# Kernel tuning notes

Measured on AMD Instinct MI355X. Metric: run time of the kernel, lower is better.

## Reference

```python
import jax, jax.numpy as jnp
import numpy as np

NUM_ENTITY = 500000
NUM_RELATION = 6000
NUM_WORD = 200000
D = 100          # entity_dim == word_dim
L = 3            # num_layer
B, E, F, Q = 16, 2000, 8000, 20
PAGERANK_LAMBDA = 0.8
FACT_SCALE = 3.0
VERY_NEG = -1e11
VERY_SMALL = 1e-10


def setup_inputs() -> dict:
    key = jax.random.key(0)
    ks = jax.random.split(key, 24)
    s = 0.05
    return {
        'local_entity': jax.random.randint(ks[0], (B, E), 0, NUM_ENTITY),
        'kb_fact_rel': jax.random.randint(ks[1], (B, F), 0, NUM_RELATION),
        'kb_head': jax.random.randint(ks[2], (B, F), 0, E),
        'kb_tail': jax.random.randint(ks[3], (B, F), 0, E),
        'query_text': jax.random.randint(ks[4], (B, Q), 0, NUM_WORD),
        'q2e_adj_mat': jax.random.uniform(ks[5], (B, E, 1)),
        'entity_table': jax.random.normal(ks[6], (NUM_ENTITY + 1, D)) * s,
        'rel_table': jax.random.normal(ks[7], (NUM_RELATION + 1, D)) * s,
        'word_table': jax.random.normal(ks[8], (NUM_WORD + 1, D)) * s,
        'rel_lin_w': jax.random.normal(ks[9], (D, D)) * s,
        'rel_lin_b': jnp.zeros((D,)),
        'lstm_wih': jax.random.normal(ks[10], (4 * D, D)) * s,
        'lstm_whh': jax.random.normal(ks[11], (4 * D, D)) * s,
        'lstm_bih': jnp.zeros((4 * D,)),
        'lstm_bhh': jnp.zeros((4 * D,)),
        'q2e_w': jax.random.normal(ks[12], (L, D, D)) * s,
        'q2e_b': jnp.zeros((L, D)),
        'e2q_w': jax.random.normal(ks[13], (L, D, 3 * D)) * s,
        'e2q_b': jnp.zeros((L, D)),
        'e2e_w': jax.random.normal(ks[14], (L, D, 3 * D)) * s,
        'e2e_b': jnp.zeros((L, D)),
        'head_w': jax.random.normal(ks[15], (L, D, D)) * s,
        'head_b': jnp.zeros((L, D)),
        'tail_w': jax.random.normal(ks[16], (L, D, D)) * s,
        'tail_b': jnp.zeros((L, D)),
        'self_w': jax.random.normal(ks[17], (L, D, D)) * s,
        'self_b': jnp.zeros((L, D)),
        'score_w': jax.random.normal(ks[18], (1, D)) * s,
        'score_b': jnp.zeros((1,)),
    }


def _lstm(x, wih, whh, bih, bhh):
    # x: (B, Q, D); torch LSTM gate order i,f,g,o
    b = x.shape[0]
    h0 = jnp.zeros((b, D), x.dtype)

    def step(carry, xt):
        h, c = carry
        g = xt @ wih.T + h @ whh.T + bih + bhh
        i, f, gg, o = jnp.split(g, 4, axis=-1)
        c = jax.nn.sigmoid(f) * c + jax.nn.sigmoid(i) * jnp.tanh(gg)
        h = jax.nn.sigmoid(o) * jnp.tanh(c)
        return (h, c), h

    (h, _), hs = jax.lax.scan(step, (h0, h0), x.transpose(1, 0, 2))
    return hs.transpose(1, 0, 2), h


def _gather(x, idx):
    # sparse_bmm(entity2fact, x): out[b,f] = x[b, head[b,f]]
    return jnp.take_along_axis(x, idx[:, :, None], axis=1)


def _scatter(x, idx, num):
    # sparse_bmm(fact2entity, x): segment-sum facts onto tail entities
    b, f, d = x.shape
    flat = (idx + jnp.arange(b)[:, None] * num).reshape(-1)
    return jax.ops.segment_sum(x.reshape(b * f, d), flat, num_segments=b * num).reshape(b, num, d)


def reference(local_entity, kb_fact_rel, kb_head, kb_tail, query_text, q2e_adj_mat,
              entity_table, rel_table, word_table, rel_lin_w, rel_lin_b,
              lstm_wih, lstm_whh, lstm_bih, lstm_bhh,
              q2e_w, q2e_b, e2q_w, e2q_b, e2e_w, e2e_b,
              head_w, head_b, tail_w, tail_b, self_w, self_b, score_w, score_b):
    div = float(np.sqrt(D))
    q_mask = (query_text != NUM_WORD).astype(jnp.float32)
    e_mask = (local_entity != NUM_ENTITY).astype(jnp.float32)

    # query LSTM encoding
    q_emb = word_table[query_text]                                   # (B,Q,D)
    q_hidden, q_last = _lstm(q_emb, lstm_wih, lstm_whh, lstm_bih, lstm_bhh)
    query_node_emb = q_last[:, None, :]                              # (B,1,D)

    # fact embeddings from relations
    fact_emb = rel_table[kb_fact_rel] @ rel_lin_w.T + rel_lin_b      # (B,F,D)

    # fact-to-query attention weights (softmax over query words)
    sim = jnp.einsum('bqd,bfd->bqf', q_hidden, fact_emb) / div
    sim = jax.nn.softmax(sim + (1.0 - q_mask)[:, :, None] * VERY_NEG, axis=1)
    att = jnp.einsum('bqf,bqd->bfd', sim, q_hidden)                  # (B,F,D)
    Wf = jnp.sum(att * fact_emb, axis=2) / div                       # (B,F)
    W_tilde = jnp.exp(Wf - Wf.max(axis=1, keepdims=True))
    e2f_softmax = jnp.clip(_scatter(W_tilde[:, :, None], kb_head, E)[:, :, 0], VERY_SMALL, None)

    local_entity_emb = entity_table[local_entity]                    # (B,E,D)
    pagerank_f = q2e_adj_mat[:, :, 0]                                # (B,E)

    for i in range(L):
        q2e_emb = jnp.broadcast_to(query_node_emb @ q2e_w[i].T + q2e_b[i], (B, E, D))
        # entity -> fact (gather heads)
        e2f = jax.nn.relu(fact_emb @ self_w[i].T + self_b[i] +
                          _gather(local_entity_emb @ head_w[i].T + head_b[i], kb_head))
        e2f = e2f * (W_tilde[:, :, None] * _gather((pagerank_f / e2f_softmax)[:, :, None], kb_head))
        # fact -> entity (scatter to tails)
        f2e = jax.nn.relu(local_entity_emb @ self_w[i].T + self_b[i] +
                          FACT_SCALE * _scatter(e2f @ tail_w[i].T + tail_b[i], kb_tail, E))
        # pagerank propagation
        pr = _scatter(_gather(pagerank_f[:, :, None], kb_head), kb_tail, E)[:, :, 0]
        pagerank_f = PAGERANK_LAMBDA * pr + (1.0 - PAGERANK_LAMBDA) * pagerank_f
        # k=3 concat -> e2q / e2e updates
        nxt = jnp.concatenate([local_entity_emb, q2e_emb, f2e], axis=2)   # (B,E,3D)
        query_node_emb = jnp.einsum('be,bed->bd', pagerank_f, nxt @ e2q_w[i].T + e2q_b[i])[:, None, :]
        local_entity_emb = jax.nn.relu(nxt @ e2e_w[i].T + e2e_b[i])

    score = (local_entity_emb @ score_w.T + score_b)[:, :, 0]
    return score + (1.0 - e_mask) * VERY_NEG
```

## Files before the change

kernel.cpp:

```cpp
#include <hip/hip_runtime.h>
#include <math.h>

namespace {

typedef unsigned short u16;
typedef short bf16x8 __attribute__((ext_vector_type(8)));
typedef float f32x4 __attribute__((ext_vector_type(4)));

constexpr int B = 16, E = 2000, F = 8000, Q = 20, D = 100, NLAYER = 3;
constexpr int NUM_ENTITY_C = 500000;
constexpr int NREL1 = 6001;
constexpr int SK = 128;
constexpr int WFSZ = 28 * 64 * 8;
constexpr int SST = 120;
constexpr float PAGERANK_LAMBDA = 0.8f;
constexpr float FACT_SCALE = 3.0f;
constexpr float VERY_NEG = -100000000000.0f;
constexpr float VERY_SMALL = 1e-10f;

__device__ __forceinline__ float sigf(float x) { return 1.0f / (1.0f + __expf(-x)); }

__device__ __forceinline__ short f2bf(float f) {
    union { float f; unsigned int u; } c; c.f = f;
    unsigned int u = c.u + 0x7FFF + ((c.u >> 16) & 1);
    return (short)(u >> 16);
}
__device__ __forceinline__ float bf2f(u16 s) {
    union { unsigned int u; float f; } c; c.u = ((unsigned int)s) << 16;
    return c.f;
}

__global__ void wprep_kernel(const float* __restrict__ rel_lin_w,
                             const float* __restrict__ self_w, const float* __restrict__ head_w,
                             const float* __restrict__ tail_w, const float* __restrict__ e2e_w,
                             u16* __restrict__ WF)
{
    int m = blockIdx.y;
    int ns = blockIdx.x;
    int n = ns >> 2, s = ns & 3;
    int lane = threadIdx.x;
    const float* W; int ldW = D, kofs = 0; float scale = 1.f;
    if (m == 0) { W = rel_lin_w; }
    else {
        int L = (m - 1) / 5, t = (m - 1) % 5;
        if (t == 0)      { W = self_w + (size_t)L * D * D; }
        else if (t == 1) { W = head_w + (size_t)L * D * D; }
        else if (t == 2) { W = tail_w + (size_t)L * D * D; scale = FACT_SCALE; }
// ... 63 lines not shown
            for (int n = 0; n < 2; ++n) {
                bf16x8 qb = *reinterpret_cast<const bf16x8*>(
                    qhB + ((size_t)(b * 8 + n * 4 + s) * 64 + lane) * 8);
                acc[n] = __builtin_amdgcn_mfma_f32_16x16x32_bf16(af[s], qb, acc[n], 0, 0, 0);
            }
        }
        const bool v1 = lrow < (Q - 16);
#pragma unroll
        for (int r = 0; r < 4; ++r) {
            float s0 = acc[0][r] * 0.1f;
            float s1 = acc[1][r] * 0.1f;
            float m = v1 ? fmaxf(s0, s1) : s0;
#pragma unroll
            for (int d = 1; d < 16; d <<= 1) m = fmaxf(m, __shfl_xor(m, d));
            float e0 = __expf(s0 - m);
            float e1 = v1 ? __expf(s1 - m) : 0.f;
            float sum = e0 + e1;
            float wsum = fmaf(e0, s0, e1 * s1);
#pragma unroll
            for (int d = 1; d < 16; d <<= 1) {
                sum += __shfl_xor(sum, d);
                wsum += __shfl_xor(wsum, d);
            }
            if (lrow == 0) {
                int orow = chunk * 16 + lkg * 4 + r;
                float wtl = __expf(wsum / sum);
                wt[orow] = wtl;
                atomicAdd(&e2fsm[headAbs[orow]], wtl);
            }
        }
    }
}

__global__ __launch_bounds__(256, 2) void mm2pipe(
    const u16* __restrict__ RELp, const int* __restrict__ srel,
    const u16* __restrict__ embp, const int* __restrict__ shead,
    const u16* __restrict__ WF1, const u16* __restrict__ WF2,
    const float* __restrict__ b1, const float* __restrict__ b2,
    const float* __restrict__ wtv, const float* __restrict__ prv,
    u16* __restrict__ outp, int nrows)
{
    __shared__ __align__(16) u16 stage[4][16][SST];
    const int lane = threadIdx.x & 63;
    const int lrow = lane & 15, lkg = lane >> 4;
    const int wslot = threadIdx.x >> 6;
    const int nch = (nrows + 15) >> 4;

    const int g = blockIdx.x & 7;
    const int lb = blockIdx.x >> 3;
    const int nchg = nch >> 3;
    const int cbase = g * nchg;
    const int wvg = lb * 4 + wslot;
    const int nwvg = 64 * 4;

    bf16x8 w1[7][4];
#pragma unroll
    for (int n = 0; n < 7; ++n)
#pragma unroll
        for (int s = 0; s < 4; ++s)
            w1[n][s] = *reinterpret_cast<const bf16x8*>(WF1 + ((size_t)(n * 4 + s) * 64 + lane) * 8);

    auto loadA = [&](int ch, bf16x8* f1, bf16x8* f2) {
        int row = ch * 16 + lrow;
        int ar = row < nrows ? row : nrows - 1;
        const u16* s1p = RELp + (size_t)srel[ar] * SK;
        const u16* s2p = embp + (size_t)shead[ar] * SK;
#pragma unroll
        for (int s = 0; s < 4; ++s) {
            f1[s] = *reinterpret_cast<const bf16x8*>(s1p + s * 32 + lkg * 8);
            f2[s] = *reinterpret_cast<const bf16x8*>(s2p + s * 32 + lkg * 8);
        }
    };

    int chunk = cbase + wvg;
    const int cend = cbase + nchg;
    if (chunk >= cend) return;
    bf16x8 cf1[4], cf2[4];
    loadA(chunk, cf1, cf2);
    while (true) {
        const int nxt = chunk + nwvg;
        const bool more = nxt < cend;
        bf16x8 nf1[4], nf2[4];
        if (more) loadA(nxt, nf1, nf2);

        f32x4 acc[7];
#pragma unroll
        for (int n = 0; n < 7; ++n) acc[n] = (f32x4){0.f, 0.f, 0.f, 0.f};
#pragma unroll
        for (int s = 0; s < 4; ++s) {
#pragma unroll
            for (int n = 0; n < 7; ++n)
                acc[n] = __builtin_amdgcn_mfma_f32_16x16x32_bf16(cf1[s], w1[n][s], acc[n], 0, 0, 0);
#pragma unroll
            for (int n = 0; n < 7; ++n) {
                bf16x8 w2 = *reinterpret_cast<const bf16x8*>(
                    WF2 + ((size_t)(n * 4 + s) * 64 + lane) * 8);
                acc[n] = __builtin_amdgcn_mfma_f32_16x16x32_bf16(cf2[s], w2, acc[n], 0, 0, 0);
            }
        }

        const int rb = chunk * 16 + lkg * 4;
#pragma unroll
        for (int r = 0; r < 4; ++r) {
            const int orow = rb + r;
            const int grow = orow < nrows ? orow : nrows - 1;
            const float rsv = wtv[grow] * prv[shead[grow]];
#pragma unroll
            for (int n = 0; n < 7; ++n) {
                const int col = n * 16 + lrow;
                float v = 0.f;
                if (col < D) {
                    v = acc[n][r] + b1[col] + b2[col];
                    v = fmaxf(v, 0.f) * rsv;
                }
                stage[wslot][lkg * 4 + r][col] = (u16)f2bf(v);
            }
        }
#pragma unroll
        for (int idx = lane; idx < 16 * 13; idx += 64) {
            int rr = idx / 13, cc = idx - rr * 13;
            int orow = chunk * 16 + rr;
            bf16x8 v = *reinterpret_cast<const bf16x8*>(&stage[wslot][rr][cc * 8]);
            if (orow < nrows)
                *reinterpret_cast<bf16x8*>(outp + (size_t)orow * SK + cc * 8) = v;
        }

        if (!more) break;
#pragma unroll
        for (int s = 0; s < 4; ++s) { cf1[s] = nf1[s]; cf2[s] = nf2[s]; }
        chunk = nxt;
    }
}

template<int A1S, int A2S, int EPI, bool OUTBF, bool PR>
__global__ __launch_bounds__(256, 2) void mm2(
    const void* __restrict__ A1p, const int* __restrict__ idx1, int lda1,
    const void* __restrict__ A2p, const int* __restrict__ idx2,
    const u16* __restrict__ WF1, const u16* __restrict__ WF2,
    const float* __restrict__ b1, const float* __restrict__ b2,
    const float* __restrict__ vq,
    const float* __restrict__ wtv, const float* __restrict__ prv,
    const int* __restrict__ row_start,
    const float* __restrict__ prOld, const int* __restrict__ sheadv,
    float* __restrict__ prNew,
    void* __restrict__ outp, int nrows)
{
    __shared__ __align__(16) u16 stage[4][16][SST];
    const int lane = threadIdx.x & 63;
    const int lrow = lane & 15, lkg = lane >> 4;
    const int wslot = threadIdx.x >> 6;
    const int wv = blockIdx.x * (blockDim.x >> 6) + wslot;
    const int nwv = gridDim.x * (blockDim.x >> 6);
    const int nch = (nrows + 15) >> 4;

    bf16x8 w1[7][4];
#pragma unroll
    for (int n = 0; n < 7; ++n)
#pragma unroll
        for (int s = 0; s < 4; ++s)
            w1[n][s] = *reinterpret_cast<const bf16x8*>(WF1 + ((size_t)(n * 4 + s) * 64 + lane) * 8);

    for (int chunk = wv; chunk < nch; chunk += nwv) {
        const int row = chunk * 16 + lrow;
        const int ar = row < nrows ? row : nrows - 1;

        bf16x8 af1[4];
        if (A1S == 0) {
            const u16* src = (const u16*)A1p + (size_t)ar * SK;
#pragma unroll
            for (int s = 0; s < 4; ++s)
                af1[s] = *reinterpret_cast<const bf16x8*>(src + s * 32 + lkg * 8);
        } else if (A1S == 1) {
            const u16* src = (const u16*)A1p + (size_t)idx1[ar] * SK;
#pragma unroll
            for (int s = 0; s < 4; ++s)
                af1[s] = *reinterpret_cast<const bf16x8*>(src + s * 32 + lkg * 8);
        } else {
            const float* arow = (const float*)A1p + (size_t)ar * lda1;
#pragma unroll
            for (int s = 0; s < 4; ++s) {
                const int k0 = s * 32 + lkg * 8;
                float tv[8];
                if (k0 + 8 <= D) {
                    float4 v0 = *reinterpret_cast<const float4*>(arow + k0);
                    float4 v1 = *reinterpret_cast<const float4*>(arow + k0 + 4);
                    tv[0]=v0.x; tv[1]=v0.y; tv[2]=v0.z; tv[3]=v0.w;
                    tv[4]=v1.x; tv[5]=v1.y; tv[6]=v1.z; tv[7]=v1.w;
                } else {
#pragma unroll
                    for (int j = 0; j < 8; ++j) tv[j] = (k0 + j < D) ? arow[k0 + j] : 0.f;
                }
                bf16x8 f;
#pragma unroll
                for (int j = 0; j < 8; ++j) f[j] = f2bf(tv[j]);
                af1[s] = f;
            }
        }

        int s0 = 0, s1 = 0;
        if (A2S == 2) { s0 = row_start[ar]; s1 = row_start[ar + 1]; }

        bf16x8 af2[4];
        if (A2S == 1) {
            const u16* src = (const u16*)A2p + (size_t)idx2[ar] * SK;
#pragma unroll
            for (int s = 0; s < 4; ++s)
                af2[s] = *reinterpret_cast<const bf16x8*>(src + s * 32 + lkg * 8);
        } else if (A2S == 3) {
            const u16* src = (const u16*)A2p + (size_t)ar * SK;
#pragma unroll
            for (int s = 0; s < 4; ++s)
                af2[s] = *reinterpret_cast<const bf16x8*>(src + s * 32 + lkg * 8);
        }

        f32x4 acc[7];
#pragma unroll
        for (int n = 0; n < 7; ++n) acc[n] = (f32x4){0.f, 0.f, 0.f, 0.f};
#pragma unroll
        for (int s = 0; s < 4; ++s) {
#pragma unroll
            for (int n = 0; n < 7; ++n)
                acc[n] = __builtin_amdgcn_mfma_f32_16x16x32_bf16(af1[s], w1[n][s], acc[n], 0, 0, 0);
            if (A2S == 1 || A2S == 3) {
#pragma unroll
                for (int n = 0; n < 7; ++n) {
                    bf16x8 w2 = *reinterpret_cast<const bf16x8*>(
                        WF2 + ((size_t)(n * 4 + s) * 64 + lane) * 8);
                    acc[n] = __builtin_amdgcn_mfma_f32_16x16x32_bf16(af2[s], w2, acc[n], 0, 0, 0);
                }
            } else if (A2S == 2) {
                float a2f[8];
#pragma unroll
                for (int j = 0; j < 8; ++j) a2f[j] = 0.f;
                for (int i = s0; i < s1; ++i) {
                    bf16x8 v = *reinterpret_cast<const bf16x8*>(
                        (const u16*)A2p + (size_t)i * SK + s * 32 + lkg * 8);
#pragma unroll
                    for (int j = 0; j < 8; ++j) a2f[j] += bf2f((u16)v[j]);
                }
                bf16x8 fsum;
#pragma unroll
                for (int j = 0; j < 8; ++j) fsum[j] = f2bf(a2f[j]);
#pragma unroll
                for (int n = 0; n < 7; ++n) {
                    bf16x8 w2 = *reinterpret_cast<const bf16x8*>(
                        WF2 + ((size_t)(n * 4 + s) * 64 + lane) * 8);
                    acc[n] = __builtin_amdgcn_mfma_f32_16x16x32_bf16(fsum, w2, acc[n], 0, 0, 0);
                }
            }
        }
        if (PR && A2S == 2) {
            if (lkg == 0 && row < nrows) {
                float a = 0.f;
                for (int i = s0; i < s1; ++i) a += prOld[sheadv[i]];
                prNew[row] = PAGERANK_LAMBDA * a + (1.0f - PAGERANK_LAMBDA) * prOld[row];
            }
        }

        const int rb = chunk * 16 + lkg * 4;
        const int bb = (chunk * 16) / E;
#pragma unroll
        for (int r = 0; r < 4; ++r) {
            const int orow = rb + r;
            const int grow = orow < nrows ? orow : nrows - 1;
            float rsv = 1.f, cntf = 0.f;
            if (EPI == 1) rsv = wtv[grow] * prv[idx2[grow]];
            if (EPI == 2) cntf = (float)(row_start[grow + 1] - row_start[grow]);
            float scr = 0.f;
#pragma unroll
            for (int n = 0; n < 7; ++n) {
                const int col = n * 16 + lrow;
                float v = 0.f;
                if (col < D) {
                    v = acc[n][r];
                    if (b1) v += b1[col];
                    if (EPI == 1) v += b2[col];
                    if (EPI == 2) v += FACT_SCALE * cntf * b2[col];
                    if (EPI == 3 || EPI == 4) v += vq[bb * D + col];
                    if (EPI != 0) v = fmaxf(v, 0.f);
                    if (EPI == 1) v *= rsv;
                }
                if (EPI == 4) {
                    if (col < D) scr = fmaf(v, b2[col], scr);
                } else if (OUTBF) {
                    stage[wslot][lkg * 4 + r][col] = (u16)f2bf(v);
                } else if (col < D && orow < nrows) {
                    ((float*)outp)[(size_t)orow * D + col] = v;
                }
            }
            if (EPI == 4) {
                scr += __shfl_xor(scr, 1);
                scr += __shfl_xor(scr, 2);
                scr += __shfl_xor(scr, 4);
                scr += __shfl_xor(scr, 8);
                if (lrow == 0 && orow < nrows) {
                    float s = scr + prOld[0] +
                              ((sheadv[orow] != NUM_ENTITY_C) ? 0.f : VERY_NEG);
                    ((float*)outp)[orow] = s;
                }
            }
        }
        if (OUTBF && EPI != 4) {
#pragma unroll
            for (int idx = lane; idx < 16 * 13; idx += 64) {
                int rr = idx / 13, cc = idx - rr * 13;
                int orow = chunk * 16 + rr;
                bf16x8 v = *reinterpret_cast<const bf16x8*>(&stage[wslot][rr][cc * 8]);
                if (orow < nrows)
                    *reinterpret_cast<bf16x8*>((u16*)outp + (size_t)orow * SK + cc * 8) = v;
            }
        }
    }
}

__global__ __launch_bounds__(512) void gatesx_kernel(
    const int* __restrict__ qtext, const float* __restrict__ wtab,
    const float* __restrict__ wih, const float* __restrict__ bih,
    const float* __restrict__ bhh, float* __restrict__ gx)
{
    int row = blockIdx.x;
    int t = threadIdx.x;
    __shared__ __align__(16) float xs[D];
    if (t < D) xs[t] = wtab[(size_t)qtext[row] * D + t];
    __syncthreads();
    if (t < 4 * D) {
        const float4* w4 = reinterpret_cast<const float4*>(wih + (size_t)t * D);
        const float4* x4 = reinterpret_cast<const float4*>(xs);
        float a0 = 0.f, a1 = 0.f, a2 = 0.f, a3 = 0.f;
#pragma unroll
        for (int k = 0; k < 25; ++k) {
            float4 wv = w4[k]; float4 xv = x4[k];
            a0 = fmaf(wv.x, xv.x, a0); a1 = fmaf(wv.y, xv.y, a1);
            a2 = fmaf(wv.z, xv.z, a2); a3 = fmaf(wv.w, xv.w, a3);
        }
        gx[(size_t)row * (4 * D) + t] = a0 + a1 + a2 + a3 + bih[t] + bhh[t];
    }
}

__global__ __launch_bounds__(512) void lstmrec_kernel(
    const float* __restrict__ gx, const float* __restrict__ whh,
    float* __restrict__ q_hidden, float* __restrict__ qne)
{
    int b = blockIdx.x, t = threadIdx.x;
// ... 5 lines not shown
        const float4* wr = reinterpret_cast<const float4*>(whh + (size_t)t * D);
#pragma unroll
        for (int k = 0; k < 25; ++k) w[k] = wr[k];
    }
    if (t < D) { h[t] = 0.f; cst[t] = 0.f; }
    __syncthreads();
    for (int step = 0; step < Q; ++step) {
        if (t < 4 * D) {
            const float4* h4 = reinterpret_cast<const float4*>(h);
            float a0 = 0.f, a1 = 0.f, a2 = 0.f, a3 = 0.f;
#pragma unroll
            for (int k = 0; k < 25; ++k) {
                float4 hv = h4[k];
                a0 = fmaf(w[k].x, hv.x, a0); a1 = fmaf(w[k].y, hv.y, a1);
                a2 = fmaf(w[k].z, hv.z, a2); a3 = fmaf(w[k].w, hv.w, a3);
            }
            g[t] = a0 + a1 + a2 + a3 + gx[((size_t)b * Q + step) * (4 * D) + t];
        }
        __syncthreads();
        if (t < D) {
            float gi = g[t], gf = g[t + D], gg = g[t + 2 * D], go = g[t + 3 * D];
            float cn = sigf(gf) * cst[t] + sigf(gi) * tanhf(gg);
            float hn = sigf(go) * tanhf(cn);
            cst[t] = cn; h[t] = hn;
            q_hidden[((size_t)b * Q + step) * D + t] = hn;
            if (step == Q - 1) qne[b * D + t] = hn;
        }
        __syncthreads();
    }
}

__global__ void idxabs_kernel(const int* __restrict__ kb_head, const int* __restrict__ kb_tail,
                              int* __restrict__ headAbs, int* __restrict__ tailAbs,
                              int* __restrict__ counts)
{
    int r = blockIdx.x * 256 + threadIdx.x;
    if (r < B * F) {
        int b = r / F;
        headAbs[r] = b * E + kb_head[r];
        int t = b * E + kb_tail[r];
        tailAbs[r] = t;
        atomicAdd(&counts[t], 1);
    }
}

__global__ __launch_bounds__(1024) void scan_kernel(const int* __restrict__ counts,
                                                    int* __restrict__ row_start,
                                                    int* __restrict__ cursor)
{
    __shared__ int part[1024];
    int t = threadIdx.x;
    int base = t * 32;
    int local[32];
    int s = 0;
#pragma unroll
    for (int i = 0; i < 32; ++i) {
        int idx = base + i;
        int v = (idx < B * E) ? counts[idx] : 0;
        local[i] = s; s += v;
    }
    part[t] = s;
    __syncthreads();
    for (int off = 1; off < 1024; off <<= 1) {
        int v = (t >= off) ? part[t - off] : 0;
        __syncthreads();
        if (t >= off) part[t] += v;
        __syncthreads();
    }
    int prev = (t > 0) ? part[t - 1] : 0;
#pragma unroll
    for (int i = 0; i < 32; ++i) {
        int idx = base + i;
        if (idx < B * E) { int rs = prev + local[i]; row_start[idx] = rs; cursor[idx] = rs; }
    }
    if (t == 1023) row_start[B * E] = part[1023];
}

__global__ void fillsprep_kernel(const int* __restrict__ tailAbs, int* __restrict__ cursor,
                                 const int* __restrict__ headAbs, const int* __restrict__ frel,
                                 const float* __restrict__ wt, const float* __restrict__ e2fsm,
                                 int* __restrict__ srel, int* __restrict__ shead,
                                 float* __restrict__ srsv)
{
    int r = blockIdx.x * 256 + threadIdx.x;
    if (r < B * F) {
        int p = atomicAdd(&cursor[tailAbs[r]], 1);
        int h = headAbs[r];
        srel[p] = frel[r];
        shead[p] = h;
        srsv[p] = wt[r] / fmaxf(e2fsm[h], VERY_SMALL);
    }
}

__global__ void entgather_kernel(const int* __restrict__ local_entity,
                                 const float* __restrict__ etab, u16* __restrict__ emb,
                                 const float* __restrict__ q2e_adj, float* __restrict__ pr)
{
    int i = blockIdx.x * 256 + threadIdx.x;
    if (i < B * E) pr[i] = q2e_adj[i];
    if (i < B * E * 25) {
        int row = i / 25, p = i - row * 25;
        float4 v = reinterpret_cast<const float4*>(etab + (size_t)local_entity[row] * D)[p];
        short4 o;
        o.x = f2bf(v.x); o.y = f2bf(v.y); o.z = f2bf(v.z); o.w = f2bf(v.w);
        *reinterpret_cast<short4*>(emb + (size_t)row * SK + p * 4) = o;
    }
}

template<bool HASQNE>
__global__ void qvec_kernel(const float* __restrict__ qneIn, float* __restrict__ z,
                            const float* __restrict__ e2qw, const float* __restrict__ e2qb,
                            const float* __restrict__ q2ew, const float* __restrict__ q2eb,
                            const float* __restrict__ e2ew,
                            float* __restrict__ q2e_vec, float* __restrict__ vq)
{
    int b = blockIdx.x, t = threadIdx.x;
    __shared__ float qn[D];
    __shared__ float qv[D];
    __shared__ float zb[201];
    float* zg = z + b * 201;
    if (HASQNE) {
        for (int i = t; i < 201; i += 128) { zb[i] = zg[i]; zg[i] = 0.f; }
        __syncthreads();
// ... 108 lines not shown
    const float* rel_table    = (const float*)d_in[7];
    const float* word_table   = (const float*)d_in[8];
    const float* rel_lin_w    = (const float*)d_in[9];
    const float* rel_lin_b    = (const float*)d_in[10];
    const float* lstm_wih     = (const float*)d_in[11];
    const float* lstm_whh     = (const float*)d_in[12];
    const float* lstm_bih     = (const float*)d_in[13];
    const float* lstm_bhh     = (const float*)d_in[14];
    const float* q2e_w        = (const float*)d_in[15];
    const float* q2e_b        = (const float*)d_in[16];
    const float* e2q_w        = (const float*)d_in[17];
    const float* e2q_b        = (const float*)d_in[18];
    const float* e2e_w        = (const float*)d_in[19];
    const float* e2e_b        = (const float*)d_in[20];
    const float* head_w       = (const float*)d_in[21];
    const float* head_b       = (const float*)d_in[22];
    const float* tail_w       = (const float*)d_in[23];
    const float* tail_b       = (const float*)d_in[24];
    const float* self_w       = (const float*)d_in[25];
    const float* self_b       = (const float*)d_in[26];
    const float* score_w      = (const float*)d_in[27];
    const float* score_b      = (const float*)d_in[28];
    float* out = (float*)d_out;

    float* ws = (float*)d_ws;
    size_t o = 0;
    auto alloc = [&](size_t n) { float* p = ws + o; o += (n + 3) & ~(size_t)3; return p; };
    float* q_hidden = alloc((size_t)B * Q * D);
    float* qne      = alloc(B * D);
    float* gx       = alloc((size_t)B * Q * 4 * D);
    float* wt       = alloc((size_t)B * F);
    float* e2fsm    = alloc(B * E);
    int*   counts   = (int*)alloc(B * E);
    float* pr0      = alloc(B * E);
    float* pr1      = alloc(B * E);
    float* q2e_vec  = alloc(B * D);
    float* vq       = alloc(B * D);
    float* z        = alloc(B * 201);
    float* srsv     = alloc((size_t)B * F);
    u16* WF   = (u16*)alloc((size_t)16 * WFSZ / 2);
    u16* qhB  = (u16*)alloc((size_t)B * 8 * 64 * 8 / 2);
    u16* REL  = (u16*)alloc((size_t)NREL1 * SK / 2 + 64);
    u16* emb0 = (u16*)alloc((size_t)B * E * SK / 2);
    u16* emb1 = (u16*)alloc((size_t)B * E * SK / 2);
    u16* e2fS = (u16*)alloc((size_t)B * F * SK / 2);
    u16* f2e  = (u16*)alloc((size_t)B * E * SK / 2);
    int* headAbs  = (int*)alloc((size_t)B * F);
    int* tailAbs  = (int*)alloc((size_t)B * F);
    int* row_start= (int*)alloc(B * E + 1);
    int* cursor   = (int*)alloc(B * E);
    int* srel     = (int*)alloc((size_t)B * F);
    int* shead    = (int*)alloc((size_t)B * F);
    if (ws_size < o * sizeof(float)) return;

    auto WFm = [&](int m) { return WF + (size_t)m * WFSZ; };

    wprep_kernel<<<dim3(28, 16), dim3(64), 0, stream>>>(rel_lin_w, self_w, head_w, tail_w,
                                                        e2e_w, WF);
    gatesx_kernel<<<dim3(B * Q), dim3(512), 0, stream>>>(query_text, word_table, lstm_wih,
                                                         lstm_bih, lstm_bhh, gx);
    lstmrec_kernel<<<dim3(B), dim3(512), 0, stream>>>(gx, lstm_whh, q_hidden, qne);
    qhprep_kernel<<<dim3(B), dim3(512), 0, stream>>>(q_hidden, qhB);
    hipMemsetAsync(e2fsm, 0, (size_t)2 * B * E * sizeof(float), stream);
    idxabs_kernel<<<dim3((B * F + 255) / 256), dim3(256), 0, stream>>>(
        kb_head, kb_tail, headAbs, tailAbs, counts);
    scan_kernel<<<dim3(1), dim3(1024), 0, stream>>>(counts, row_start, cursor);
    mm2<2, 0, 0, true, false><<<dim3(mmgrid(NREL1)), dim3(256), 0, stream>>>(
        rel_table, nullptr, D, nullptr, nullptr, WFm(0), nullptr, rel_lin_b, nullptr,
        nullptr, nullptr, nullptr, nullptr, nullptr, nullptr, nullptr,
        REL, NREL1);
    wfm_kernel<<<dim3(mmgrid2(B * F)), dim3(256), 0, stream>>>(
        REL, kb_fact_rel, qhB, headAbs, wt, e2fsm, B * F);
    fillsprep_kernel<<<dim3((B * F + 255) / 256), dim3(256), 0, stream>>>(
        tailAbs, cursor, headAbs, kb_fact_rel, wt, e2fsm, srel, shead, srsv);
    entgather_kernel<<<dim3((B * E * 25 + 255) / 256), dim3(256), 0, stream>>>(
        local_entity, entity_table, emb0, q2e_adj, pr0);

    u16* embO = emb0; u16* embN = emb1;
    float* prO = pr0; float* prN = pr1;
    for (int i = 0; i < NLAYER; ++i) {
        const float* q2e_wi  = q2e_w + (size_t)i * D * D;
        const float* q2e_bi  = q2e_b + i * D;
        const float* e2e_wi  = e2e_w + (size_t)i * D * 3 * D;
        const float* e2e_bi  = e2e_b + i * D;
        const float* head_bi = head_b + i * D;
        const float* tail_bi = tail_b + i * D;
        const float* self_bi = self_b + i * D;
        const u16* wf_self = WFm(1 + i * 5 + 0);
        const u16* wf_head = WFm(1 + i * 5 + 1);
        const u16* wf_tail = WFm(1 + i * 5 + 2);
        const u16* wf_e2e0 = WFm(1 + i * 5 + 3);
        const u16* wf_e2e2 = WFm(1 + i * 5 + 4);
        const bool last = (i == NLAYER - 1);

        if (i == 0)
            qvec_kernel<false><<<dim3(B), dim3(128), 0, stream>>>(
                qne, z, nullptr, nullptr, q2e_wi, q2e_bi, e2e_wi, q2e_vec, vq);
        else
            qvec_kernel<true><<<dim3(B), dim3(128), 0, stream>>>(
                nullptr, z, e2q_w + (size_t)(i - 1) * D * 3 * D, e2q_b + (size_t)(i - 1) * D,
                q2e_wi, q2e_bi, e2e_wi, q2e_vec, vq);

        mm2pipe<<<dim3(512), dim3(256), 0, stream>>>(
            REL, srel, embO, shead, wf_self, wf_head, self_bi, head_bi,
            srsv, prO, e2fS, B * F);
        if (!last)
            mm2<0, 2, 2, true, true><<<dim3(mmgrid(B * E)), dim3(256), 0, stream>>>(
                embO, nullptr, 0, e2fS, nullptr, wf_self, wf_tail, self_bi, tail_bi,
                nullptr, nullptr, nullptr, row_start, prO, shead, prN,
                f2e, B * E);
        else
            mm2<0, 2, 2, true, false><<<dim3(mmgrid(B * E)), dim3(256), 0, stream>>>(
                embO, nullptr, 0, e2fS, nullptr, wf_self, wf_tail, self_bi, tail_bi,
                nullptr, nullptr, nullptr, row_start, nullptr, nullptr, nullptr,
                f2e, B * E);
        if (!last)
            zsum_kernel<<<dim3(B, 16), dim3(256), 0, stream>>>(prN, embO, f2e, z);
        if (!last)
            mm2<0, 3, 3, true, false><<<dim3(mmgrid(B * E)), dim3(256), 0, stream>>>(
                embO, nullptr, 0, f2e, nullptr, wf_e2e0, wf_e2e2, e2e_bi, nullptr,
                vq, nullptr, nullptr, nullptr, nullptr, nullptr, nullptr,
                embN, B * E);
        else
            mm2<0, 3, 4, false, false><<<dim3(mmgrid(B * E)), dim3(256), 0, stream>>>(
                embO, nullptr, 0, f2e, nullptr, wf_e2e0, wf_e2e2, e2e_bi, score_w,
                vq, nullptr, nullptr, nullptr, score_b, local_entity, nullptr,
                out, B * E);
        { u16* tmp = embO; embO = embN; embN = tmp; }
        { float* tmp = prO; prO = prN; prN = tmp; }
    }
}
```

Measured before the change: 559.1 us.

## Fuse fact-to-entity matmul with e2e update matmul per row chunk

```diff
diff --git a/kernel.cpp b/kernel.cpp
--- a/kernel.cpp
+++ b/kernel.cpp
@@ -13,6 +13,7 @@
 constexpr int SK = 128;
 constexpr int WFSZ = 28 * 64 * 8;
 constexpr int SST = 120;
+constexpr int SST2 = 136;
 constexpr float PAGERANK_LAMBDA = 0.8f;
 constexpr float FACT_SCALE = 3.0f;
 constexpr float VERY_NEG = -100000000000.0f;
@@ -242,25 +243,26 @@
     }
 }
 
-template<int A1S, int A2S, int EPI, bool OUTBF, bool PR>
-__global__ __launch_bounds__(256, 2) void mm2(
-    const void* __restrict__ A1p, const int* __restrict__ idx1, int lda1,
-    const void* __restrict__ A2p, const int* __restrict__ idx2,
-    const u16* __restrict__ WF1, const u16* __restrict__ WF2,
-    const float* __restrict__ b1, const float* __restrict__ b2,
-    const float* __restrict__ vq,
-    const float* __restrict__ wtv, const float* __restrict__ prv,
+template<bool LASTL>
+__global__ __launch_bounds__(256, 2) void mm2ef(
+    const u16* __restrict__ embp, const u16* __restrict__ e2fSp,
+    const u16* __restrict__ WFself, const u16* __restrict__ WFtail,
+    const u16* __restrict__ WFe0, const u16* __restrict__ WFe2,
+    const float* __restrict__ self_b, const float* __restrict__ tail_b,
+    const float* __restrict__ e2e_b, const float* __restrict__ vq,
     const int* __restrict__ row_start,
     const float* __restrict__ prOld, const int* __restrict__ sheadv,
     float* __restrict__ prNew,
-    void* __restrict__ outp, int nrows)
-{
-    __shared__ __align__(16) u16 stage[4][16][SST];
+    u16* __restrict__ f2ep, void* __restrict__ outp,
+    const float* __restrict__ score_w, const float* __restrict__ score_b,
+    const int* __restrict__ le, int nrows)
+{
+    __shared__ __align__(16) u16 stage[4][16][SST2];
     const int lane = threadIdx.x & 63;
     const int lrow = lane & 15, lkg = lane >> 4;
     const int wslot = threadIdx.x >> 6;
-    const int wv = blockIdx.x * (blockDim.x >> 6) + wslot;
-    const int nwv = gridDim.x * (blockDim.x >> 6);
+    const int wv = blockIdx.x * 4 + wslot;
+    const int nwv = gridDim.x * 4;
     const int nch = (nrows + 15) >> 4;
 
     bf16x8 w1[7][4];
@@ -268,60 +270,21 @@
     for (int n = 0; n < 7; ++n)
 #pragma unroll
         for (int s = 0; s < 4; ++s)
-            w1[n][s] = *reinterpret_cast<const bf16x8*>(WF1 + ((size_t)(n * 4 + s) * 64 + lane) * 8);
+            w1[n][s] = *reinterpret_cast<const bf16x8*>(WFself + ((size_t)(n * 4 + s) * 64 + lane) * 8);
 
     for (int chunk = wv; chunk < nch; chunk += nwv) {
         const int row = chunk * 16 + lrow;
         const int ar = row < nrows ? row : nrows - 1;
+        const int bb = (chunk * 16) / E;
 
         bf16x8 af1[4];
-        if (A1S == 0) {
-            const u16* src = (const u16*)A1p + (size_t)ar * SK;
+        {
+            const u16* src = embp + (size_t)ar * SK;
 #pragma unroll
             for (int s = 0; s < 4; ++s)
                 af1[s] = *reinterpret_cast<const bf16x8*>(src + s * 32 + lkg * 8);
-        } else if (A1S == 1) {
-            const u16* src = (const u16*)A1p + (size_t)idx1[ar] * SK;
-#pragma unroll
-            for (int s = 0; s < 4; ++s)
-                af1[s] = *reinterpret_cast<const bf16x8*>(src + s * 32 + lkg * 8);
-        } else {
-            const float* arow = (const float*)A1p + (size_t)ar * lda1;
-#pragma unroll
-            for (int s = 0; s < 4; ++s) {
-                const int k0 = s * 32 + lkg * 8;
-                float tv[8];
-                if (k0 + 8 <= D) {
-                    float4 v0 = *reinterpret_cast<const float4*>(arow + k0);
-                    float4 v1 = *reinterpret_cast<const float4*>(arow + k0 + 4);
-                    tv[0]=v0.x; tv[1]=v0.y; tv[2]=v0.z; tv[3]=v0.w;
-                    tv[4]=v1.x; tv[5]=v1.y; tv[6]=v1.z; tv[7]=v1.w;
-                } else {
-#pragma unroll
-                    for (int j = 0; j < 8; ++j) tv[j] = (k0 + j < D) ? arow[k0 + j] : 0.f;
-                }
-                bf16x8 f;
-#pragma unroll
-                for (int j = 0; j < 8; ++j) f[j] = f2bf(tv[j]);
-                af1[s] = f;
-            }
-        }
-
-        int s0 = 0, s1 = 0;
-        if (A2S == 2) { s0 = row_start[ar]; s1 = row_start[ar + 1]; }
-
-        bf16x8 af2[4];
-        if (A2S == 1) {
-            const u16* src = (const u16*)A2p + (size_t)idx2[ar] * SK;
-#pragma unroll
-            for (int s = 0; s < 4; ++s)
-                af2[s] = *reinterpret_cast<const bf16x8*>(src + s * 32 + lkg * 8);
-        } else if (A2S == 3) {
-            const u16* src = (const u16*)A2p + (size_t)ar * SK;
-#pragma unroll
-            for (int s = 0; s < 4; ++s)
-                af2[s] = *reinterpret_cast<const bf16x8*>(src + s * 32 + lkg * 8);
-        }
+        }
+        const int s0 = row_start[ar], s1 = row_start[ar + 1];
 
         f32x4 acc[7];
 #pragma unroll
@@ -331,35 +294,26 @@
 #pragma unroll
             for (int n = 0; n < 7; ++n)
                 acc[n] = __builtin_amdgcn_mfma_f32_16x16x32_bf16(af1[s], w1[n][s], acc[n], 0, 0, 0);
-            if (A2S == 1 || A2S == 3) {
-#pragma unroll
-                for (int n = 0; n < 7; ++n) {
-                    bf16x8 w2 = *reinterpret_cast<const bf16x8*>(
-                        WF2 + ((size_t)(n * 4 + s) * 64 + lane) * 8);
-                    acc[n] = __builtin_amdgcn_mfma_f32_16x16x32_bf16(af2[s], w2, acc[n], 0, 0, 0);
-                }
-            } else if (A2S == 2) {
-                float a2f[8];
-#pragma unroll
-                for (int j = 0; j < 8; ++j) a2f[j] = 0.f;
-                for (int i = s0; i < s1; ++i) {
-                    bf16x8 v = *reinterpret_cast<const bf16x8*>(
-                        (const u16*)A2p + (size_t)i * SK + s * 32 + lkg * 8);
-#pragma unroll
-                    for (int j = 0; j < 8; ++j) a2f[j] += bf2f((u16)v[j]);
-                }
-                bf16x8 fsum;
-#pragma unroll
-                for (int j = 0; j < 8; ++j) fsum[j] = f2bf(a2f[j]);
-#pragma unroll
-                for (int n = 0; n < 7; ++n) {
-                    bf16x8 w2 = *reinterpret_cast<const bf16x8*>(
-                        WF2 + ((size_t)(n * 4 + s) * 64 + lane) * 8);
-                    acc[n] = __builtin_amdgcn_mfma_f32_16x16x32_bf16(fsum, w2, acc[n], 0, 0, 0);
-                }
-            }
-        }
-        if (PR && A2S == 2) {
+            float a2f[8];
+#pragma unroll
+            for (int j = 0; j < 8; ++j) a2f[j] = 0.f;
+            for (int i = s0; i < s1; ++i) {
+                bf16x8 v = *reinterpret_cast<const bf16x8*>(
+                    e2fSp + (size_t)i * SK + s * 32 + lkg * 8);
+#pragma unroll
+                for (int j = 0; j < 8; ++j) a2f[j] += bf2f((u16)v[j]);
+            }
+            bf16x8 fsum;
+#pragma unroll
+            for (int j = 0; j < 8; ++j) fsum[j] = f2bf(a2f[j]);
+#pragma unroll
+            for (int n = 0; n < 7; ++n) {
+                bf16x8 w2 = *reinterpret_cast<const bf16x8*>(
+                    WFtail + ((size_t)(n * 4 + s) * 64 + lane) * 8);
+                acc[n] = __builtin_amdgcn_mfma_f32_16x16x32_bf16(fsum, w2, acc[n], 0, 0, 0);
+            }
+        }
+        if (!LASTL) {
             if (lkg == 0 && row < nrows) {
                 float a = 0.f;
                 for (int i = s0; i < s1; ++i) a += prOld[sheadv[i]];
@@ -368,49 +322,87 @@
         }
 
         const int rb = chunk * 16 + lkg * 4;
-        const int bb = (chunk * 16) / E;
 #pragma unroll
         for (int r = 0; r < 4; ++r) {
             const int orow = rb + r;
             const int grow = orow < nrows ? orow : nrows - 1;
-            float rsv = 1.f, cntf = 0.f;
-            if (EPI == 1) rsv = wtv[grow] * prv[idx2[grow]];
-            if (EPI == 2) cntf = (float)(row_start[grow + 1] - row_start[grow]);
-            float scr = 0.f;
+            const float cntf = (float)(row_start[grow + 1] - row_start[grow]);
 #pragma unroll
             for (int n = 0; n < 7; ++n) {
                 const int col = n * 16 + lrow;
                 float v = 0.f;
                 if (col < D) {
-                    v = acc[n][r];
-                    if (b1) v += b1[col];
-                    if (EPI == 1) v += b2[col];
-                    if (EPI == 2) v += FACT_SCALE * cntf * b2[col];
-                    if (EPI == 3 || EPI == 4) v += vq[bb * D + col];
-                    if (EPI != 0) v = fmaxf(v, 0.f);
-                    if (EPI == 1) v *= rsv;
+                    v = acc[n][r] + self_b[col] + FACT_SCALE * cntf * tail_b[col];
+                    v = fmaxf(v, 0.f);
                 }
-                if (EPI == 4) {
-                    if (col < D) scr = fmaf(v, b2[col], scr);
-                } else if (OUTBF) {
+                stage[wslot][lkg * 4 + r][col] = (u16)f2bf(v);
+            }
+            stage[wslot][lkg * 4 + r][112 + lrow] = 0;
+        }
+#pragma unroll
+        for (int idx = lane; idx < 16 * 13; idx += 64) {
+            int rr = idx / 13, cc = idx - rr * 13;
+            int orow = chunk * 16 + rr;
+            bf16x8 v = *reinterpret_cast<const bf16x8*>(&stage[wslot][rr][cc * 8]);
+            if (orow < nrows)
+                *reinterpret_cast<bf16x8*>(f2ep + (size_t)orow * SK + cc * 8) = v;
+        }
+
+        bf16x8 ff[4];
+#pragma unroll
+        for (int s = 0; s < 4; ++s)
+            ff[s] = *reinterpret_cast<const bf16x8*>(&stage[wslot][lrow][s * 32 + lkg * 8]);
+
+        f32x4 acc2[7];
+#pragma unroll
+        for (int n = 0; n < 7; ++n) acc2[n] = (f32x4){0.f, 0.f, 0.f, 0.f};
+#pragma unroll
+        for (int s = 0; s < 4; ++s) {
+#pragma unroll
+            for (int n = 0; n < 7; ++n) {
+                bf16x8 w0 = *reinterpret_cast<const bf16x8*>(
+                    WFe0 + ((size_t)(n * 4 + s) * 64 + lane) * 8);
+                acc2[n] = __builtin_amdgcn_mfma_f32_16x16x32_bf16(af1[s], w0, acc2[n], 0, 0, 0);
+            }
+#pragma unroll
+            for (int n = 0; n < 7; ++n) {
+                bf16x8 w2 = *reinterpret_cast<const bf16x8*>(
+                    WFe2 + ((size_t)(n * 4 + s) * 64 + lane) * 8);
+                acc2[n] = __builtin_amdgcn_mfma_f32_16x16x32_bf16(ff[s], w2, acc2[n], 0, 0, 0);
+            }
+        }
+
+#pragma unroll
+        for (int r = 0; r < 4; ++r) {
+            const int orow = rb + r;
+            float scr = 0.f;
+#pragma unroll
+            for (int n = 0; n < 7; ++n) {
+                const int col = n * 16 + lrow;
+                float v = 0.f;
+                if (col < D) {
+                    v = acc2[n][r] + e2e_b[col] + vq[bb * D + col];
+                    v = fmaxf(v, 0.f);
+                }
+                if (LASTL) {
+                    if (col < D) scr = fmaf(v, score_w[col], scr);
+                } else {
                     stage[wslot][lkg * 4 + r][col] = (u16)f2bf(v);
-                } else if (col < D && orow < nrows) {
-                    ((float*)outp)[(size_t)orow * D + col] = v;
                 }
             }
-            if (EPI == 4) {
+            if (LASTL) {
                 scr += __shfl_xor(scr, 1);
                 scr += __shfl_xor(scr, 2);
                 scr += __shfl_xor(scr, 4);
                 scr += __shfl_xor(scr, 8);
                 if (lrow == 0 && orow < nrows) {
-                    float s = scr + prOld[0] +
-                              ((sheadv[orow] != NUM_ENTITY_C) ? 0.f : VERY_NEG);
+                    float s = scr + score_b[0] +
+                              ((le[orow] != NUM_ENTITY_C) ? 0.f : VERY_NEG);
                     ((float*)outp)[orow] = s;
                 }
             }
         }
-        if (OUTBF && EPI != 4) {
+        if (!LASTL) {
 #pragma unroll
             for (int idx = lane; idx < 16 * 13; idx += 64) {
                 int rr = idx / 13, cc = idx - rr * 13;
@@ -419,6 +411,80 @@
                 if (orow < nrows)
                     *reinterpret_cast<bf16x8*>((u16*)outp + (size_t)orow * SK + cc * 8) = v;
             }
+        }
+    }
+}
+
+__global__ __launch_bounds__(256, 2) void mmrel(
+    const float* __restrict__ A1p, int lda1,
+    const u16* __restrict__ WF1, const float* __restrict__ b1,
+    u16* __restrict__ outp, int nrows)
+{
+    __shared__ __align__(16) u16 stage[4][16][SST];
+    const int lane = threadIdx.x & 63;
+    const int lrow = lane & 15, lkg = lane >> 4;
+    const int wslot = threadIdx.x >> 6;
+    const int wv = blockIdx.x * 4 + wslot;
+    const int nwv = gridDim.x * 4;
+    const int nch = (nrows + 15) >> 4;
+
+    bf16x8 w1[7][4];
+#pragma unroll
+    for (int n = 0; n < 7; ++n)
+#pragma unroll
+        for (int s = 0; s < 4; ++s)
+            w1[n][s] = *reinterpret_cast<const bf16x8*>(WF1 + ((size_t)(n * 4 + s) * 64 + lane) * 8);
+
+    for (int chunk = wv; chunk < nch; chunk += nwv) {
+        const int row = chunk * 16 + lrow;
+        const int ar = row < nrows ? row : nrows - 1;
+        bf16x8 af1[4];
+        const float* arow = A1p + (size_t)ar * lda1;
+#pragma unroll
+        for (int s = 0; s < 4; ++s) {
+            const int k0 = s * 32 + lkg * 8;
+            float tv[8];
+            if (k0 + 8 <= D) {
+                float4 v0 = *reinterpret_cast<const float4*>(arow + k0);
+                float4 v1 = *reinterpret_cast<const float4*>(arow + k0 + 4);
+                tv[0]=v0.x; tv[1]=v0.y; tv[2]=v0.z; tv[3]=v0.w;
+                tv[4]=v1.x; tv[5]=v1.y; tv[6]=v1.z; tv[7]=v1.w;
+            } else {
+#pragma unroll
+                for (int j = 0; j < 8; ++j) tv[j] = (k0 + j < D) ? arow[k0 + j] : 0.f;
+            }
+            bf16x8 f;
+#pragma unroll
+            for (int j = 0; j < 8; ++j) f[j] = f2bf(tv[j]);
+            af1[s] = f;
+        }
+
+        f32x4 acc[7];
+#pragma unroll
+        for (int n = 0; n < 7; ++n) acc[n] = (f32x4){0.f, 0.f, 0.f, 0.f};
+#pragma unroll
+        for (int s = 0; s < 4; ++s)
+#pragma unroll
+            for (int n = 0; n < 7; ++n)
+                acc[n] = __builtin_amdgcn_mfma_f32_16x16x32_bf16(af1[s], w1[n][s], acc[n], 0, 0, 0);
+
+#pragma unroll
+        for (int r = 0; r < 4; ++r) {
+#pragma unroll
+            for (int n = 0; n < 7; ++n) {
+                const int col = n * 16 + lrow;
+                float v = 0.f;
+                if (col < D) v = acc[n][r] + b1[col];
+                stage[wslot][lkg * 4 + r][col] = (u16)f2bf(v);
+            }
+        }
+#pragma unroll
+        for (int idx = lane; idx < 16 * 13; idx += 64) {
+            int rr = idx / 13, cc = idx - rr * 13;
+            int orow = chunk * 16 + rr;
+            bf16x8 v = *reinterpret_cast<const bf16x8*>(&stage[wslot][rr][cc * 8]);
+            if (orow < nrows)
+                *reinterpret_cast<bf16x8*>(outp + (size_t)orow * SK + cc * 8) = v;
         }
     }
 }
@@ -754,10 +820,8 @@
     idxabs_kernel<<<dim3((B * F + 255) / 256), dim3(256), 0, stream>>>(
         kb_head, kb_tail, headAbs, tailAbs, counts);
     scan_kernel<<<dim3(1), dim3(1024), 0, stream>>>(counts, row_start, cursor);
-    mm2<2, 0, 0, true, false><<<dim3(mmgrid(NREL1)), dim3(256), 0, stream>>>(
-        rel_table, nullptr, D, nullptr, nullptr, WFm(0), nullptr, rel_lin_b, nullptr,
-        nullptr, nullptr, nullptr, nullptr, nullptr, nullptr, nullptr,
-        REL, NREL1);
+    mmrel<<<dim3(mmgrid(NREL1)), dim3(256), 0, stream>>>(
+        rel_table, D, WFm(0), rel_lin_b, REL, NREL1);
     wfm_kernel<<<dim3(mmgrid2(B * F)), dim3(256), 0, stream>>>(
         REL, kb_fact_rel, qhB, headAbs, wt, e2fsm, B * F);
     fillsprep_kernel<<<dim3((B * F + 255) / 256), dim3(256), 0, stream>>>(
@@ -794,27 +858,17 @@
             REL, srel, embO, shead, wf_self, wf_head, self_bi, head_bi,
             srsv, prO, e2fS, B * F);
         if (!last)
-            mm2<0, 2, 2, true, true><<<dim3(mmgrid(B * E)), dim3(256), 0, stream>>>(
-                embO, nullptr, 0, e2fS, nullptr, wf_self, wf_tail, self_bi, tail_bi,
-                nullptr, nullptr, nullptr, row_start, prO, shead, prN,
-                f2e, B * E);
+            mm2ef<false><<<dim3(mmgrid(B * E)), dim3(256), 0, stream>>>(
+                embO, e2fS, wf_self, wf_tail, wf_e2e0, wf_e2e2,
+                self_bi, tail_bi, e2e_bi, vq, row_start, prO, shead, prN,
+                f2e, embN, nullptr, nullptr, nullptr, B * E);
         else
-            mm2<0, 2, 2, true, false><<<dim3(mmgrid(B * E)), dim3(256), 0, stream>>>(
-                embO, nullptr, 0, e2fS, nullptr, wf_self, wf_tail, self_bi, tail_bi,
-                nullptr, nullptr, nullptr, row_start, nullptr, nullptr, nullptr,
-                f2e, B * E);
+            mm2ef<true><<<dim3(mmgrid(B * E)), dim3(256), 0, stream>>>(
+                embO, e2fS, wf_self, wf_tail, wf_e2e0, wf_e2e2,
+                self_bi, tail_bi, e2e_bi, vq, row_start, prO, shead, nullptr,
+                f2e, out, score_w, score_b, local_entity, B * E);
         if (!last)
             zsum_kernel<<<dim3(B, 16), dim3(256), 0, stream>>>(prN, embO, f2e, z);
-        if (!last)
-            mm2<0, 3, 3, true, false><<<dim3(mmgrid(B * E)), dim3(256), 0, stream>>>(
-                embO, nullptr, 0, f2e, nullptr, wf_e2e0, wf_e2e2, e2e_bi, nullptr,
-                vq, nullptr, nullptr, nullptr, nullptr, nullptr, nullptr,
-                embN, B * E);
-        else
-            mm2<0, 3, 4, false, false><<<dim3(mmgrid(B * E)), dim3(256), 0, stream>>>(
-                embO, nullptr, 0, f2e, nullptr, wf_e2e0, wf_e2e2, e2e_bi, score_w,
-                vq, nullptr, nullptr, nullptr, score_b, local_entity, nullptr,
-                out, B * E);
         { u16* tmp = embO; embO = embN; embN = tmp; }
         { float* tmp = prO; prO = prN; prN = tmp; }
     }
```

Result: slower. 763.5 us (+36.6%).

## Process facts in head-sorted order and scatter results to tail-sorted positions

Applied to the files above, without the earlier changes.

```diff
diff --git a/kernel.cpp b/kernel.cpp
--- a/kernel.cpp
+++ b/kernel.cpp
@@ -142,15 +142,17 @@
     }
 }
 
-__global__ __launch_bounds__(256, 2) void mm2pipe(
-    const u16* __restrict__ RELp, const int* __restrict__ srel,
-    const u16* __restrict__ embp, const int* __restrict__ shead,
+__global__ __launch_bounds__(256, 2) void mm2pipeH(
+    const u16* __restrict__ RELp, const int* __restrict__ hrel,
+    const u16* __restrict__ embp, const int* __restrict__ hhead,
+    const int* __restrict__ houtpos,
     const u16* __restrict__ WF1, const u16* __restrict__ WF2,
     const float* __restrict__ b1, const float* __restrict__ b2,
-    const float* __restrict__ wtv, const float* __restrict__ prv,
+    const float* __restrict__ hrsv, const float* __restrict__ prv,
     u16* __restrict__ outp, int nrows)
 {
     __shared__ __align__(16) u16 stage[4][16][SST];
+    __shared__ int opos[4][16];
     const int lane = threadIdx.x & 63;
     const int lrow = lane & 15, lkg = lane >> 4;
     const int wslot = threadIdx.x >> 6;
@@ -173,8 +175,8 @@
     auto loadA = [&](int ch, bf16x8* f1, bf16x8* f2) {
         int row = ch * 16 + lrow;
         int ar = row < nrows ? row : nrows - 1;
-        const u16* s1p = RELp + (size_t)srel[ar] * SK;
-        const u16* s2p = embp + (size_t)shead[ar] * SK;
+        const u16* s1p = RELp + (size_t)hrel[ar] * SK;
+        const u16* s2p = embp + (size_t)hhead[ar] * SK;
 #pragma unroll
         for (int s = 0; s < 4; ++s) {
             f1[s] = *reinterpret_cast<const bf16x8*>(s1p + s * 32 + lkg * 8);
@@ -212,9 +214,9 @@
         const int rb = chunk * 16 + lkg * 4;
 #pragma unroll
         for (int r = 0; r < 4; ++r) {
-            const int orow = rb + r;
-            const int grow = orow < nrows ? orow : nrows - 1;
-            const float rsv = wtv[grow] * prv[shead[grow]];
+            const int irow = rb + r;
+            const int grow = irow < nrows ? irow : nrows - 1;
+            const float rsv = hrsv[grow] * prv[hhead[grow]];
 #pragma unroll
             for (int n = 0; n < 7; ++n) {
                 const int col = n * 16 + lrow;
@@ -225,13 +227,14 @@
                 }
                 stage[wslot][lkg * 4 + r][col] = (u16)f2bf(v);
             }
+            if (lrow == 0) opos[wslot][lkg * 4 + r] = (irow < nrows) ? houtpos[irow] : -1;
         }
 #pragma unroll
         for (int idx = lane; idx < 16 * 13; idx += 64) {
             int rr = idx / 13, cc = idx - rr * 13;
-            int orow = chunk * 16 + rr;
+            int orow = opos[wslot][rr];
             bf16x8 v = *reinterpret_cast<const bf16x8*>(&stage[wslot][rr][cc * 8]);
-            if (orow < nrows)
+            if (orow >= 0)
                 *reinterpret_cast<bf16x8*>(outp + (size_t)orow * SK + cc * 8) = v;
         }
 
@@ -244,12 +247,11 @@
 
 template<int A1S, int A2S, int EPI, bool OUTBF, bool PR>
 __global__ __launch_bounds__(256, 2) void mm2(
-    const void* __restrict__ A1p, const int* __restrict__ idx1, int lda1,
-    const void* __restrict__ A2p, const int* __restrict__ idx2,
+    const void* __restrict__ A1p, int lda1,
+    const void* __restrict__ A2p,
     const u16* __restrict__ WF1, const u16* __restrict__ WF2,
     const float* __restrict__ b1, const float* __restrict__ b2,
     const float* __restrict__ vq,
-    const float* __restrict__ wtv, const float* __restrict__ prv,
     const int* __restrict__ row_start,
     const float* __restrict__ prOld, const int* __restrict__ sheadv,
     float* __restrict__ prNew,
@@ -277,11 +279,6 @@
         bf16x8 af1[4];
         if (A1S == 0) {
             const u16* src = (const u16*)A1p + (size_t)ar * SK;
-#pragma unroll
-            for (int s = 0; s < 4; ++s)
-                af1[s] = *reinterpret_cast<const bf16x8*>(src + s * 32 + lkg * 8);
-        } else if (A1S == 1) {
-            const u16* src = (const u16*)A1p + (size_t)idx1[ar] * SK;
 #pragma unroll
             for (int s = 0; s < 4; ++s)
                 af1[s] = *reinterpret_cast<const bf16x8*>(src + s * 32 + lkg * 8);
@@ -311,16 +308,11 @@
         if (A2S == 2) { s0 = row_start[ar]; s1 = row_start[ar + 1]; }
 
         bf16x8 af2[4];
-        if (A2S == 1) {
-            const u16* src = (const u16*)A2p + (size_t)idx2[ar] * SK;
+        if (A2S == 3) {
+            const u16* src = (const u16*)A2p + (size_t)ar * SK;
 #pragma unroll
             for (int s = 0; s < 4; ++s)
                 af2[s] = *reinterpret_cast<const bf16x8*>(src + s * 32 + lkg * 8);
-        } else if (A2S == 3) {
-            const u16* src = (const u16*)A2p + (size_t)ar * SK;
-#pragma unroll
-            for (int s = 0; s < 4; ++s)
-                af2[s] = *reinterpret_cast<const bf16x8*>(src + s * 32 + lkg * 8);
         }
 
         f32x4 acc[7];
@@ -331,7 +323,7 @@
 #pragma unroll
             for (int n = 0; n < 7; ++n)
                 acc[n] = __builtin_amdgcn_mfma_f32_16x16x32_bf16(af1[s], w1[n][s], acc[n], 0, 0, 0);
-            if (A2S == 1 || A2S == 3) {
+            if (A2S == 3) {
 #pragma unroll
                 for (int n = 0; n < 7; ++n) {
                     bf16x8 w2 = *reinterpret_cast<const bf16x8*>(
@@ -373,8 +365,7 @@
         for (int r = 0; r < 4; ++r) {
             const int orow = rb + r;
             const int grow = orow < nrows ? orow : nrows - 1;
-            float rsv = 1.f, cntf = 0.f;
-            if (EPI == 1) rsv = wtv[grow] * prv[idx2[grow]];
+            float cntf = 0.f;
             if (EPI == 2) cntf = (float)(row_start[grow + 1] - row_start[grow]);
             float scr = 0.f;
 #pragma unroll
@@ -384,11 +375,9 @@
                 if (col < D) {
                     v = acc[n][r];
                     if (b1) v += b1[col];
-                    if (EPI == 1) v += b2[col];
                     if (EPI == 2) v += FACT_SCALE * cntf * b2[col];
                     if (EPI == 3 || EPI == 4) v += vq[bb * D + col];
                     if (EPI != 0) v = fmaxf(v, 0.f);
-                    if (EPI == 1) v *= rsv;
                 }
                 if (EPI == 4) {
                     if (col < D) scr = fmaf(v, b2[col], scr);
@@ -490,15 +479,17 @@
 
 __global__ void idxabs_kernel(const int* __restrict__ kb_head, const int* __restrict__ kb_tail,
                               int* __restrict__ headAbs, int* __restrict__ tailAbs,
-                              int* __restrict__ counts)
+                              int* __restrict__ counts, int* __restrict__ hcounts)
 {
     int r = blockIdx.x * 256 + threadIdx.x;
     if (r < B * F) {
         int b = r / F;
-        headAbs[r] = b * E + kb_head[r];
+        int h = b * E + kb_head[r];
+        headAbs[r] = h;
         int t = b * E + kb_tail[r];
         tailAbs[r] = t;
         atomicAdd(&counts[t], 1);
+        atomicAdd(&hcounts[h], 1);
     }
 }
 
@@ -535,18 +526,23 @@
 }
 
 __global__ void fillsprep_kernel(const int* __restrict__ tailAbs, int* __restrict__ cursor,
+                                 int* __restrict__ hcursor,
                                  const int* __restrict__ headAbs, const int* __restrict__ frel,
                                  const float* __restrict__ wt, const float* __restrict__ e2fsm,
-                                 int* __restrict__ srel, int* __restrict__ shead,
-                                 float* __restrict__ srsv)
+                                 int* __restrict__ shead,
+                                 int* __restrict__ hrel, int* __restrict__ hhead,
+                                 float* __restrict__ hrsv, int* __restrict__ houtpos)
 {
     int r = blockIdx.x * 256 + threadIdx.x;
     if (r < B * F) {
+        int h = headAbs[r];
         int p = atomicAdd(&cursor[tailAbs[r]], 1);
-        int h = headAbs[r];
-        srel[p] = frel[r];
         shead[p] = h;
-        srsv[p] = wt[r] / fmaxf(e2fsm[h], VERY_SMALL);
+        int p2 = atomicAdd(&hcursor[h], 1);
+        hrel[p2] = frel[r];
+        hhead[p2] = h;
+        hrsv[p2] = wt[r] / fmaxf(e2fsm[h], VERY_SMALL);
+        houtpos[p2] = p;
     }
 }
 
@@ -721,12 +717,13 @@
     float* wt       = alloc((size_t)B * F);
     float* e2fsm    = alloc(B * E);
     int*   counts   = (int*)alloc(B * E);
+    int*   hcounts  = (int*)alloc(B * E);
     float* pr0      = alloc(B * E);
     float* pr1      = alloc(B * E);
     float* q2e_vec  = alloc(B * D);
     float* vq       = alloc(B * D);
     float* z        = alloc(B * 201);
-    float* srsv     = alloc((size_t)B * F);
+    float* hrsv     = alloc((size_t)B * F);
     u16* WF   = (u16*)alloc((size_t)16 * WFSZ / 2);
     u16* qhB  = (u16*)alloc((size_t)B * 8 * 64 * 8 / 2);
     u16* REL  = (u16*)alloc((size_t)NREL1 * SK / 2 + 64);
@@ -737,9 +734,13 @@
     int* headAbs  = (int*)alloc((size_t)B * F);
     int* tailAbs  = (int*)alloc((size_t)B * F);
     int* row_start= (int*)alloc(B * E + 1);
+    int* hstart   = (int*)alloc(B * E + 1);
     int* cursor   = (int*)alloc(B * E);
-    int* srel     = (int*)alloc((size_t)B * F);
+    int* hcursor  = (int*)alloc(B * E);
     int* shead    = (int*)alloc((size_t)B * F);
+    int* hrel     = (int*)alloc((size_t)B * F);
+    int* hhead    = (int*)alloc((size_t)B * F);
+    int* houtpos  = (int*)alloc((size_t)B * F);
     if (ws_size < o * sizeof(float)) return;
 
     auto WFm = [&](int m) { return WF + (size_t)m * WFSZ; };
@@ -750,18 +751,20 @@
                                                          lstm_bih, lstm_bhh, gx);
     lstmrec_kernel<<<dim3(B), dim3(512), 0, stream>>>(gx, lstm_whh, q_hidden, qne);
     qhprep_kernel<<<dim3(B), dim3(512), 0, stream>>>(q_hidden, qhB);
-    hipMemsetAsync(e2fsm, 0, (size_t)2 * B * E * sizeof(float), stream);
+    hipMemsetAsync(e2fsm, 0, (size_t)3 * B * E * sizeof(float), stream);
     idxabs_kernel<<<dim3((B * F + 255) / 256), dim3(256), 0, stream>>>(
-        kb_head, kb_tail, headAbs, tailAbs, counts);
+        kb_head, kb_tail, headAbs, tailAbs, counts, hcounts);
     scan_kernel<<<dim3(1), dim3(1024), 0, stream>>>(counts, row_start, cursor);
+    scan_kernel<<<dim3(1), dim3(1024), 0, stream>>>(hcounts, hstart, hcursor);
     mm2<2, 0, 0, true, false><<<dim3(mmgrid(NREL1)), dim3(256), 0, stream>>>(
-        rel_table, nullptr, D, nullptr, nullptr, WFm(0), nullptr, rel_lin_b, nullptr,
-        nullptr, nullptr, nullptr, nullptr, nullptr, nullptr, nullptr,
+        rel_table, D, nullptr, WFm(0), nullptr, rel_lin_b, nullptr,
+        nullptr, nullptr, nullptr, nullptr, nullptr,
         REL, NREL1);
     wfm_kernel<<<dim3(mmgrid2(B * F)), dim3(256), 0, stream>>>(
         REL, kb_fact_rel, qhB, headAbs, wt, e2fsm, B * F);
     fillsprep_kernel<<<dim3((B * F + 255) / 256), dim3(256), 0, stream>>>(
-        tailAbs, cursor, headAbs, kb_fact_rel, wt, e2fsm, srel, shead, srsv);
+        tailAbs, cursor, hcursor, headAbs, kb_fact_rel, wt, e2fsm,
+        shead, hrel, hhead, hrsv, houtpos);
     entgather_kernel<<<dim3((B * E * 25 + 255) / 256), dim3(256), 0, stream>>>(
         local_entity, entity_table, emb0, q2e_adj, pr0);
 
@@ -790,30 +793,30 @@
                 nullptr, z, e2q_w + (size_t)(i - 1) * D * 3 * D, e2q_b + (size_t)(i - 1) * D,
                 q2e_wi, q2e_bi, e2e_wi, q2e_vec, vq);
 
-        mm2pipe<<<dim3(512), dim3(256), 0, stream>>>(
-            REL, srel, embO, shead, wf_self, wf_head, self_bi, head_bi,
-            srsv, prO, e2fS, B * F);
+        mm2pipeH<<<dim3(512), dim3(256), 0, stream>>>(
+            REL, hrel, embO, hhead, houtpos, wf_self, wf_head, self_bi, head_bi,
+            hrsv, prO, e2fS, B * F);
         if (!last)
             mm2<0, 2, 2, true, true><<<dim3(mmgrid(B * E)), dim3(256), 0, stream>>>(
-                embO, nullptr, 0, e2fS, nullptr, wf_self, wf_tail, self_bi, tail_bi,
-                nullptr, nullptr, nullptr, row_start, prO, shead, prN,
+                embO, 0, e2fS, wf_self, wf_tail, self_bi, tail_bi,
+                nullptr, row_start, prO, shead, prN,
                 f2e, B * E);
         else
             mm2<0, 2, 2, true, false><<<dim3(mmgrid(B * E)), dim3(256), 0, stream>>>(
-                embO, nullptr, 0, e2fS, nullptr, wf_self, wf_tail, self_bi, tail_bi,
-                nullptr, nullptr, nullptr, row_start, nullptr, nullptr, nullptr,
+                embO, 0, e2fS, wf_self, wf_tail, self_bi, tail_bi,
+                nullptr, row_start, nullptr, nullptr, nullptr,
                 f2e, B * E);
         if (!last)
             zsum_kernel<<<dim3(B, 16), dim3(256), 0, stream>>>(prN, embO, f2e, z);
         if (!last)
             mm2<0, 3, 3, true, false><<<dim3(mmgrid(B * E)), dim3(256), 0, stream>>>(
-                embO, nullptr, 0, f2e, nullptr, wf_e2e0, wf_e2e2, e2e_bi, nullptr,
-                vq, nullptr, nullptr, nullptr, nullptr, nullptr, nullptr,
+                embO, 0, f2e, wf_e2e0, wf_e2e2, e2e_bi, nullptr,
+                vq, nullptr, nullptr, nullptr, nullptr,
                 embN, B * E);
         else
             mm2<0, 3, 4, false, false><<<dim3(mmgrid(B * E)), dim3(256), 0, stream>>>(
-                embO, nullptr, 0, f2e, nullptr, wf_e2e0, wf_e2e2, e2e_bi, score_w,
-                vq, nullptr, nullptr, nullptr, score_b, local_entity, nullptr,
+                embO, 0, f2e, wf_e2e0, wf_e2e2, e2e_bi, score_w,
+                vq, nullptr, score_b, local_entity, nullptr,
                 out, B * E);
         { u16* tmp = embO; embO = embN; embN = tmp; }
         { float* tmp = prO; prO = prN; prN = tmp; }
```

Result: slower. 630.4 us (+12.7%).
